# Kernel optimization log

Measured on AMD Instinct MI355X. Metric: run time of the kernel, lower is better.

The kernel has to match this reference:

```python
import jax, jax.numpy as jnp
import numpy as np

B, C_IN, C_OUT, N, K = 1, 64, 64, 50000, 20


def setup_inputs() -> dict:
    key = jax.random.key(0)
    k1, k2, k3, k4, k5 = jax.random.split(key, 5)
    x = jax.random.normal(k1, (B, C_IN, N, 1), dtype=jnp.float32)
    edge_index = jax.random.randint(k2, (2, B, N, K), 0, N, dtype=jnp.int64)
    dis = jax.random.uniform(k3, (B, N, K), dtype=jnp.float32)
    W = jax.random.normal(k4, (C_OUT, 2 * C_IN), dtype=jnp.float32) * (2.0 / (2 * C_IN)) ** 0.5
    b = jnp.zeros((C_OUT,), dtype=jnp.float32)
    att_w = jax.random.normal(k5, (K,), dtype=jnp.float32) * (2.0 / K) ** 0.5
    att_b = jnp.zeros((1,), dtype=jnp.float32)
    return {"x": x, "edge_index": edge_index, "dis": dis, "W": W, "b": b,
            "att_w": att_w, "att_b": att_b}


def reference(x, edge_index, dis, W, b, att_w, att_b):
    # x: [B, C, N, 1]; edge_index: [2, B, N, K]; dis: [B, N, K]
    x2 = x[..., 0]  # [B, C, N]
    gather = jax.vmap(lambda xb, ib: xb[:, ib])  # per-batch: [C,N] idx[N,K] -> [C,N,K]
    x_i = gather(x2, edge_index[1])  # [B, C, N, K]
    x_j = gather(x2, edge_index[0])  # [B, C, N, K]
    feat = jnp.concatenate([x_i, x_j - x_i], axis=1)  # [B, 2C, N, K]
    # 1x1 conv == channel contraction
    feat = jax.nn.relu(jnp.einsum('oc,bcnk->bonk', W, feat) + b[None, :, None, None])
    # attention over the k channel of dis -> per-node scaler
    scaler = jnp.tanh(jnp.einsum('k,bnk->bn', att_w, dis) + att_b) + 1.0  # [B, N]
    suppression = 2.0 * jax.nn.sigmoid(-dis * scaler[:, :, None])  # [B, N, K]
    feat = feat * suppression[:, None, :, :]  # [B, C_out, N, K]
    return jnp.max(feat, axis=-1, keepdims=True)  # [B, C_out, N, 1]
```

## Files before the change

### kernel.cpp

```cpp
#include <hip/hip_runtime.h>

#define NN 50000
#define KK 20

__device__ __align__(256) ushort g_pool[2][2][NN * 32];
__device__ __align__(256) float  g_sup[NN * KK];

static __device__ __forceinline__ ushort f2bf(float f) {
    unsigned int u = __float_as_uint(f);
    unsigned int r = (u + 0x7FFFu + ((u >> 16) & 1u)) >> 16;
    return (ushort)r;
}
static __device__ __forceinline__ float bfl(unsigned int u) {
    return __uint_as_float(u << 16);
}
static __device__ __forceinline__ float bfh(unsigned int u) {
    return __uint_as_float(u & 0xffff0000u);
}

__global__ __launch_bounds__(256) void prep_kernel(
    const float* __restrict__ x,
    const float* __restrict__ W,
    const float* __restrict__ b,
    const float* __restrict__ dis,
    const float* __restrict__ att_w,
    const float* __restrict__ att_b)
{
    __shared__ float At[64][66];
    __shared__ float Bt[64][66];
    __shared__ float xt[64][132];
    __shared__ float disL[128 * KK];
    __shared__ float scalerL[128];

    const int t  = threadIdx.x;
    const int n0 = blockIdx.x * 128;

    for (int i = t; i < 64 * 64; i += 256) {
        int c = i >> 6, ci = i & 63;
        float w1 = W[c * 128 + ci];
        float w2 = W[c * 128 + 64 + ci];
        At[ci][c] = w1 - w2;
        Bt[ci][c] = w2;
    }
    {
        const int q  = t & 31;
        const int cb = t >> 5;
        const float4* x4 = (const float4*)x;
        const int nq = (n0 >> 2) + q;
        #pragma unroll
        for (int i = 0; i < 8; i++) {
            const int ci = cb * 8 + i;
            float4 v = (nq < 12500) ? x4[ci * 12500 + nq]
                                    : float4{0.f, 0.f, 0.f, 0.f};
            *(float4*)&xt[ci][q * 4] = v;
        }
    }
    for (int i = t; i < 128 * KK; i += 256) {
        const int gi = n0 * KK + i;
        disL[i] = (gi < NN * KK) ? dis[gi] : 0.f;
    }
    __syncthreads();

    if (t < 128) {
        float z = att_b[0];
        #pragma unroll
        for (int k = 0; k < KK; k++) z += att_w[k] * disL[t * KK + k];
        scalerL[t] = 2.f / (1.f + __expf(-2.f * z));
    }
    __syncthreads();

    for (int i = t; i < 128 * KK; i += 256) {
        const int gi = n0 * KK + i;
        if (gi < NN * KK)
            g_sup[gi] = 2.f / (1.f + __expf(disL[i] * scalerL[i / KK]));
    }

    const int c2 = t & 31;
    const int g  = t >> 5;

    float aA0[16], aA1[16], aB0[16], aB1[16];
    #pragma unroll
    for (int j = 0; j < 16; j++) { aA0[j]=0.f; aA1[j]=0.f; aB0[j]=0.f; aB1[j]=0.f; }

    for (int ci = 0; ci < 64; ci++) {
        const float2 a  = *(const float2*)&At[ci][c2 * 2];
        const float2 w2 = *(const float2*)&Bt[ci][c2 * 2];
        const float4* xr = (const float4*)&xt[ci][g * 16];
        #pragma unroll
        for (int q = 0; q < 4; q++) {
            float4 xv = xr[q];
            aA0[q*4+0] += a.x*xv.x;  aA1[q*4+0] += a.y*xv.x;
            aB0[q*4+0] += w2.x*xv.x; aB1[q*4+0] += w2.y*xv.x;
            aA0[q*4+1] += a.x*xv.y;  aA1[q*4+1] += a.y*xv.y;
            aB0[q*4+1] += w2.x*xv.y; aB1[q*4+1] += w2.y*xv.y;
            aA0[q*4+2] += a.x*xv.z;  aA1[q*4+2] += a.y*xv.z;
            aB0[q*4+2] += w2.x*xv.z; aB1[q*4+2] += w2.y*xv.z;
            aA0[q*4+3] += a.x*xv.w;  aA1[q*4+3] += a.y*xv.w;
            aB0[q*4+3] += w2.x*xv.w; aB1[q*4+3] += w2.y*xv.w;
        }
    }

    const float b0 = b[c2 * 2], b1 = b[c2 * 2 + 1];
    const int gq = c2 >> 4;
    const int pp = c2 & 15;
    unsigned int* poolU = (unsigned int*)g_pool;
    const size_t pa = (size_t)(gq * 2 + 0) * NN * 16;
    const size_t pb = (size_t)(gq * 2 + 1) * NN * 16;
    #pragma unroll
    for (int j = 0; j < 16; j++) {
        const int n = n0 + g * 16 + j;
        if (n < NN) {
            poolU[pa + (size_t)n * 16 + pp] = (unsigned int)f2bf(aA0[j] + b0)
                                            | ((unsigned int)f2bf(aA1[j] + b1) << 16);
            poolU[pb + (size_t)n * 16 + pp] = (unsigned int)f2bf(aB0[j])
                                            | ((unsigned int)f2bf(aB1[j]) << 16);
        }
    }
}

__global__ __launch_bounds__(256) void edge_kernel(
    const int* __restrict__ ej,
    const int* __restrict__ ei,
    float* __restrict__ out)
{
    __shared__ float tile[40][36];

    const int t    = threadIdx.x;
    const int lane = t & 63;
    const int w    = t >> 6;
    const int slot = lane >> 3;
    const int q    = lane & 7;
    const int bx   = blockIdx.x;
    const int grp  = bx & 1;
    const int n0   = (bx >> 1) * 40;
    const int nb   = n0 + w * 10;

    const char* pA = (const char*)&g_pool[grp][0][0];
    const char* pB = (const char*)&g_pool[grp][1][0];

    int offI[10], offJ[10]; float sup10[10];
    #pragma unroll
    for (int s = 0; s < 10; s++) {
        const int n = nb + s;
        int ii = 0, jj = 0; float sp = 0.f;
        if (lane < KK) {
            ii = __builtin_nontemporal_load(&ei[n * KK + lane]);
            jj = __builtin_nontemporal_load(&ej[n * KK + lane]);
            sp = __builtin_nontemporal_load(&g_sup[n * KK + lane]);
        }
        offI[s] = ii << 6;
        offJ[s] = jj << 6;
        sup10[s] = sp;
    }

    #pragma unroll
    for (int s = 0; s < 10; s++) {
        float4 m = {0.f, 0.f, 0.f, 0.f};
        #pragma unroll
        for (int r = 0; r < 3; r++) {
            const int   src = r * 8 + slot;
            const int   oi  = __shfl(offI[s], src);
            const int   oj  = __shfl(offJ[s], src);
            const float sp  = __shfl(sup10[s], src);
            const uint2 a   = *(const uint2*)(pA + oi + q * 8);
            const uint2 bb  = *(const uint2*)(pB + oj + q * 8);
            m.x = fmaxf(m.x, (bfl(a.x) + bfl(bb.x)) * sp);
            m.y = fmaxf(m.y, (bfh(a.x) + bfh(bb.x)) * sp);
            m.z = fmaxf(m.z, (bfl(a.y) + bfl(bb.y)) * sp);
            m.w = fmaxf(m.w, (bfh(a.y) + bfh(bb.y)) * sp);
        }
        #pragma unroll
        for (int mask = 8; mask <= 32; mask <<= 1) {
            m.x = fmaxf(m.x, __shfl_xor(m.x, mask));
            m.y = fmaxf(m.y, __shfl_xor(m.y, mask));
            m.z = fmaxf(m.z, __shfl_xor(m.z, mask));
            m.w = fmaxf(m.w, __shfl_xor(m.w, mask));
        }
        if (slot == 0) *(float4*)&tile[w * 10 + s][q * 4] = m;
    }
    __syncthreads();

    #pragma unroll
    for (int cn = 0; cn < 5; cn++) {
        const int c  = t >> 3;
        const int nl = cn * 8 + (t & 7);
        __builtin_nontemporal_store(tile[nl][c],
                                    &out[(size_t)(grp * 32 + c) * NN + n0 + nl]);
    }
}

extern "C" void kernel_launch(void* const* d_in, const int* in_sizes, int n_in,
                              void* d_out, int out_size, void* d_ws, size_t ws_size,
                              hipStream_t stream) {
    const float* x     = (const float*)d_in[0];
    const int*   e     = (const int*)d_in[1];
    const float* dis   = (const float*)d_in[2];
    const float* W     = (const float*)d_in[3];
    const float* b     = (const float*)d_in[4];
    const float* att_w = (const float*)d_in[5];
    const float* att_b = (const float*)d_in[6];
    float* out = (float*)d_out;

    (void)d_ws; (void)ws_size;

    prep_kernel<<<(NN + 127) / 128, 256, 0, stream>>>(x, W, b, dis, att_w, att_b);
    edge_kernel<<<2 * (NN / 40), 256, 0, stream>>>(e, e + NN * KK, out);
}
```

Baseline: 145.9 us.

## Stage edge indices in shared memory and use 16-byte neighbor gathers

The edge kernel now loads each block's neighbor offsets and suppression weights cooperatively into shared memory, instead of per-wave registers broadcast with shuffles. Each neighbor row is then gathered by four lanes with 16-byte loads rather than eight lanes with 8-byte loads. Each iteration handles two nodes with 32 padded neighbor slots, which is meant to raise memory-level parallelism and cut shuffle traffic for index broadcast. In exchange it adds wasted padded-slot loads and a longer cross-lane max reduction over more values.

```diff
diff --git a/kernel.cpp b/kernel.cpp
--- a/kernel.cpp
+++ b/kernel.cpp
@@ -123,60 +123,93 @@
     const int* __restrict__ ei,
     float* __restrict__ out)
 {
+    __shared__ uint2 ijL[40][32];
+    __shared__ float supL[40][32];
     __shared__ float tile[40][36];
 
     const int t    = threadIdx.x;
     const int lane = t & 63;
     const int w    = t >> 6;
-    const int slot = lane >> 3;
-    const int q    = lane & 7;
+    const int slot = lane >> 2;
+    const int q    = lane & 3;
     const int bx   = blockIdx.x;
     const int grp  = bx & 1;
     const int n0   = (bx >> 1) * 40;
-    const int nb   = n0 + w * 10;
+
+    for (int i = t; i < 40 * 32; i += 256) {
+        const int s = i >> 5, se = i & 31;
+        uint2 o = {0u, 0u}; float sp = 0.f;
+        if (se < KK) {
+            const int n = n0 + s;
+            o.x = ((unsigned)__builtin_nontemporal_load(&ei[n * KK + se])) << 6;
+            o.y = ((unsigned)__builtin_nontemporal_load(&ej[n * KK + se])) << 6;
+            sp  = __builtin_nontemporal_load(&g_sup[n * KK + se]);
+        }
+        ijL[s][se]  = o;
+        supL[s][se] = sp;
+    }
+    __syncthreads();
 
     const char* pA = (const char*)&g_pool[grp][0][0];
     const char* pB = (const char*)&g_pool[grp][1][0];
 
-    int offI[10], offJ[10]; float sup10[10];
-    #pragma unroll
-    for (int s = 0; s < 10; s++) {
-        const int n = nb + s;
-        int ii = 0, jj = 0; float sp = 0.f;
-        if (lane < KK) {
-            ii = __builtin_nontemporal_load(&ei[n * KK + lane]);
-            jj = __builtin_nontemporal_load(&ej[n * KK + lane]);
-            sp = __builtin_nontemporal_load(&g_sup[n * KK + lane]);
-        }
-        offI[s] = ii << 6;
-        offJ[s] = jj << 6;
-        sup10[s] = sp;
-    }
-
-    #pragma unroll
-    for (int s = 0; s < 10; s++) {
-        float4 m = {0.f, 0.f, 0.f, 0.f};
-        #pragma unroll
-        for (int r = 0; r < 3; r++) {
-            const int   src = r * 8 + slot;
-            const int   oi  = __shfl(offI[s], src);
-            const int   oj  = __shfl(offJ[s], src);
-            const float sp  = __shfl(sup10[s], src);
-            const uint2 a   = *(const uint2*)(pA + oi + q * 8);
-            const uint2 bb  = *(const uint2*)(pB + oj + q * 8);
-            m.x = fmaxf(m.x, (bfl(a.x) + bfl(bb.x)) * sp);
-            m.y = fmaxf(m.y, (bfh(a.x) + bfh(bb.x)) * sp);
-            m.z = fmaxf(m.z, (bfl(a.y) + bfl(bb.y)) * sp);
-            m.w = fmaxf(m.w, (bfh(a.y) + bfh(bb.y)) * sp);
-        }
-        #pragma unroll
-        for (int mask = 8; mask <= 32; mask <<= 1) {
-            m.x = fmaxf(m.x, __shfl_xor(m.x, mask));
-            m.y = fmaxf(m.y, __shfl_xor(m.y, mask));
-            m.z = fmaxf(m.z, __shfl_xor(m.z, mask));
-            m.w = fmaxf(m.w, __shfl_xor(m.w, mask));
-        }
-        if (slot == 0) *(float4*)&tile[w * 10 + s][q * 4] = m;
+    #pragma unroll 1
+    for (int s2 = 0; s2 < 5; s2++) {
+        const int r0 = w * 10 + s2 * 2;
+        const int r1 = r0 + 1;
+
+        const uint2 eA0 = ijL[r0][slot];
+        const uint2 eA1 = ijL[r0][16 + slot];
+        const uint2 eB0 = ijL[r1][slot];
+        const uint2 eB1 = ijL[r1][16 + slot];
+        const float sA0 = supL[r0][slot];
+        const float sA1 = supL[r0][16 + slot];
+        const float sB0 = supL[r1][slot];
+        const float sB1 = supL[r1][16 + slot];
+
+        const uint4 a00 = *(const uint4*)(pA + eA0.x + q * 16);
+        const uint4 b00 = *(const uint4*)(pB + eA0.y + q * 16);
+        const uint4 a01 = *(const uint4*)(pA + eA1.x + q * 16);
+        const uint4 b01 = *(const uint4*)(pB + eA1.y + q * 16);
+        const uint4 a10 = *(const uint4*)(pA + eB0.x + q * 16);
+        const uint4 b10 = *(const uint4*)(pB + eB0.y + q * 16);
+        const uint4 a11 = *(const uint4*)(pA + eB1.x + q * 16);
+        const uint4 b11 = *(const uint4*)(pB + eB1.y + q * 16);
+
+        float m0[8], m1[8];
+        #pragma unroll
+        for (int i = 0; i < 8; i++) { m0[i] = 0.f; m1[i] = 0.f; }
+
+#define ACC(m, a, bb, sp)                                          \
+        m[0] = fmaxf(m[0], (bfl(a.x) + bfl(bb.x)) * sp);           \
+        m[1] = fmaxf(m[1], (bfh(a.x) + bfh(bb.x)) * sp);           \
+        m[2] = fmaxf(m[2], (bfl(a.y) + bfl(bb.y)) * sp);           \
+        m[3] = fmaxf(m[3], (bfh(a.y) + bfh(bb.y)) * sp);           \
+        m[4] = fmaxf(m[4], (bfl(a.z) + bfl(bb.z)) * sp);           \
+        m[5] = fmaxf(m[5], (bfh(a.z) + bfh(bb.z)) * sp);           \
+        m[6] = fmaxf(m[6], (bfl(a.w) + bfl(bb.w)) * sp);           \
+        m[7] = fmaxf(m[7], (bfh(a.w) + bfh(bb.w)) * sp);
+
+        ACC(m0, a00, b00, sA0)
+        ACC(m0, a01, b01, sA1)
+        ACC(m1, a10, b10, sB0)
+        ACC(m1, a11, b11, sB1)
+#undef ACC
+
+        #pragma unroll
+        for (int mask = 4; mask <= 32; mask <<= 1) {
+            #pragma unroll
+            for (int i = 0; i < 8; i++) {
+                m0[i] = fmaxf(m0[i], __shfl_xor(m0[i], mask));
+                m1[i] = fmaxf(m1[i], __shfl_xor(m1[i], mask));
+            }
+        }
+        if (slot == 0) {
+            *(float4*)&tile[r0][q * 8]     = float4{m0[0], m0[1], m0[2], m0[3]};
+            *(float4*)&tile[r0][q * 8 + 4] = float4{m0[4], m0[5], m0[6], m0[7]};
+            *(float4*)&tile[r1][q * 8]     = float4{m1[0], m1[1], m1[2], m1[3]};
+            *(float4*)&tile[r1][q * 8 + 4] = float4{m1[4], m1[5], m1[6], m1[7]};
+        }
     }
     __syncthreads();
 
```

Measured after the change: 150.7 us. 3.3% more time.
